# Optimization experiments

Hardware: AMD Instinct MI355X
Metric: run time of the kernel (lower is better)

## Reference

```python
import jax, jax.numpy as jnp
import numpy as np

N_NODES, N_EDGES, BATCH = 50000, 100000, 256
H = 64            # dim_hidden_features
D_NODE, D_EDGE, D_RBF = 110, 8, 8
D_SET = 2 * H     # Set2Set input_dim = 128, output_dim = 256
D_HID = 512
D_CAT = 54
MP_STEPS, S2S_ITERS = 4, 3


def setup_inputs() -> dict:
    key = jax.random.key(0)
    ks = iter(jax.random.split(key, 48))

    def nrm(shape, s=0.05):
        return jax.random.normal(next(ks), shape, dtype=jnp.float32) * s

    inp = {}
    inp["node_attribute"] = jax.random.normal(next(ks), (N_NODES, D_NODE), dtype=jnp.float32)
    inp["edge_attribute"] = jax.random.normal(next(ks), (N_EDGES, D_EDGE), dtype=jnp.float32)
    inp["edge_length"] = jax.random.uniform(next(ks), (N_EDGES,), dtype=jnp.float32)
    inp["src"] = jax.random.randint(next(ks), (N_EDGES,), 0, N_NODES, dtype=jnp.int32)
    inp["dst"] = jax.random.randint(next(ks), (N_EDGES,), 0, N_NODES, dtype=jnp.int32)
    inp["node_graph"] = jnp.sort(jax.random.randint(next(ks), (N_NODES,), 0, BATCH, dtype=jnp.int32))
    # atom_feature_projector
    inp["proj_W"] = nrm((D_NODE, H)); inp["proj_b"] = jnp.zeros((H,), jnp.float32)
    # RBF layer: centers ~ U(0,1), beta = 10 (per reset_parameters)
    inp["centers"] = jax.random.uniform(next(ks), (D_RBF,), dtype=jnp.float32)
    inp["beta"] = jnp.full((D_RBF,), 10.0, jnp.float32)
    # NNConv edge function: Linear(16 -> 64*64), plus NNConv bias
    inp["bond_W"] = nrm((D_EDGE + D_RBF, H * H)); inp["bond_b"] = jnp.zeros((H * H,), jnp.float32)
    inp["conv_b"] = jnp.zeros((H,), jnp.float32)
    # GRU (input H, hidden H); PyTorch layout (3H, in)
    inp["gru_Wih"] = nrm((3 * H, H)); inp["gru_Whh"] = nrm((3 * H, H))
    inp["gru_bih"] = jnp.zeros((3 * H,), jnp.float32); inp["gru_bhh"] = jnp.zeros((3 * H,), jnp.float32)
    # Set2Set LSTM: input 2*D_SET=256, hidden D_SET=128, 2 layers; PyTorch layout (4H, in)
    inp["lstm_Wih0"] = nrm((4 * D_SET, 2 * D_SET)); inp["lstm_Whh0"] = nrm((4 * D_SET, D_SET))
    inp["lstm_bih0"] = jnp.zeros((4 * D_SET,), jnp.float32); inp["lstm_bhh0"] = jnp.zeros((4 * D_SET,), jnp.float32)
    inp["lstm_Wih1"] = nrm((4 * D_SET, D_SET)); inp["lstm_Whh1"] = nrm((4 * D_SET, D_SET))
    inp["lstm_bih1"] = jnp.zeros((4 * D_SET,), jnp.float32); inp["lstm_bhh1"] = jnp.zeros((4 * D_SET,), jnp.float32)
    # sparsify: Linear(256 -> 512) + PReLU(init 0.25)
    inp["sp_W"] = nrm((2 * D_SET, D_HID)); inp["sp_b"] = jnp.zeros((D_HID,), jnp.float32)
    inp["prelu_a"] = jnp.array([0.25], jnp.float32)
    # catalyst1 head: hiddens[0] (512->512 ReLU, 512->512 Tanh) then outputs[0] (512->54)
    inp["h0_W1"] = nrm((D_HID, D_HID)); inp["h0_b1"] = jnp.zeros((D_HID,), jnp.float32)
    inp["h0_W2"] = nrm((D_HID, D_HID)); inp["h0_b2"] = jnp.zeros((D_HID,), jnp.float32)
    inp["out_W"] = nrm((D_HID, D_CAT)); inp["out_b"] = jnp.zeros((D_CAT,), jnp.float32)
    return inp


def _lstm_cell(x, h, c, Wih, Whh, bih, bhh):
    # PyTorch LSTM gate order: i, f, g, o
    g = x @ Wih.T + bih + h @ Whh.T + bhh
    i, f, gg, o = jnp.split(g, 4, axis=-1)
    c = jax.nn.sigmoid(f) * c + jax.nn.sigmoid(i) * jnp.tanh(gg)
    h = jax.nn.sigmoid(o) * jnp.tanh(c)
    return h, c


def reference(node_attribute, edge_attribute, edge_length, src, dst, node_graph,
              proj_W, proj_b, centers, beta, bond_W, bond_b, conv_b,
              gru_Wih, gru_Whh, gru_bih, gru_bhh,
              lstm_Wih0, lstm_Whh0, lstm_bih0, lstm_bhh0,
              lstm_Wih1, lstm_Whh1, lstm_bih1, lstm_bhh1,
              sp_W, sp_b, prelu_a, h0_W1, h0_b1, h0_W2, h0_b2, out_W, out_b):
    n_nodes = node_attribute.shape[0]
    # atom feature projection
    x = jax.nn.relu(node_attribute @ proj_W + proj_b)                       # (N, H)
    # edge features = [edge_attribute, RBF(length)]
    rbf = jnp.exp(-beta * (edge_length[:, None] - centers[None, :]) ** 2)   # (E, 8)
    efeat = jnp.concatenate([edge_attribute, rbf], axis=-1)                 # (E, 16)
    # NNConv per-edge weight matrix; edge features are constant over MP steps
    W_e = (efeat @ bond_W + bond_b).reshape(-1, H, H)                       # (E, H, H)

    feat, h = x, x
    for _ in range(MP_STEPS):
        # NNConv: message = h_src @ W_e, sum-aggregated at dst, plus bias
        m = jnp.einsum('ei,eio->eo', feat[src], W_e)                        # (E, H)
        agg = jax.ops.segment_sum(m, dst, num_segments=n_nodes) + conv_b    # (N, H)
        gx = jax.nn.relu(agg)
        # GRU cell (PyTorch gate order r, z, n)
        gi = gx @ gru_Wih.T + gru_bih
        gh = h @ gru_Whh.T + gru_bhh
        i_r, i_z, i_n = jnp.split(gi, 3, axis=-1)
        h_r, h_z, h_n = jnp.split(gh, 3, axis=-1)
        r = jax.nn.sigmoid(i_r + h_r)
        z = jax.nn.sigmoid(i_z + h_z)
        n = jnp.tanh(i_n + r * h_n)
        h = (1.0 - z) * n + z * h
        feat = h
    node_agg = jnp.concatenate([feat, x], axis=-1)                          # (N, 2H)

    # Set2Set pooling over graphs (segment softmax attention, 2-layer LSTM)
    B = BATCH
    h0 = c0 = jnp.zeros((B, D_SET), node_agg.dtype)
    h1 = c1 = jnp.zeros((B, D_SET), node_agg.dtype)
    q_star = jnp.zeros((B, 2 * D_SET), node_agg.dtype)
    for _ in range(S2S_ITERS):
        h0, c0 = _lstm_cell(q_star, h0, c0, lstm_Wih0, lstm_Whh0, lstm_bih0, lstm_bhh0)
        h1, c1 = _lstm_cell(h0, h1, c1, lstm_Wih1, lstm_Whh1, lstm_bih1, lstm_bhh1)
        q = h1                                                              # (B, 128)
        e = jnp.sum(node_agg * q[node_graph], axis=-1)                      # (N,)
        emax = jax.ops.segment_max(e, node_graph, num_segments=B)
        p = jnp.exp(e - emax[node_graph])
        denom = jax.ops.segment_sum(p, node_graph, num_segments=B)
        alpha = p / denom[node_graph]                                       # per-graph softmax
        r_out = jax.ops.segment_sum(node_agg * alpha[:, None], node_graph, num_segments=B)
        q_star = jnp.concatenate([q, r_out], axis=-1)                       # (B, 256)

    # sparsify (Linear + PReLU)
    feats = q_star @ sp_W + sp_b                                            # (B, 512)
    feats = jnp.where(feats >= 0, feats, prelu_a * feats)
    # catalyst1 head
    hid = jnp.tanh(jax.nn.relu(feats @ h0_W1 + h0_b1) @ h0_W2 + h0_b2)
    return jax.nn.softmax(hid @ out_W + out_b, axis=-1)                     # (B, 54)
```

## Files before the change

kernel.cpp:

```cpp
#include <hip/hip_runtime.h>
#include <math.h>

constexpr int N = 50000;
constexpr int E = 100000;
constexpr int B = 256;
constexpr int H = 64;
constexpr int DN = 110;
constexpr int NBLK = (E + 63) / 64;

#define DEV __device__ __forceinline__

typedef __attribute__((ext_vector_type(8))) short short8;
typedef __attribute__((ext_vector_type(4))) float floatx4;

DEV float sigf(float x) { return 1.0f / (1.0f + expf(-x)); }

DEV short f2bf(float f) {
    unsigned u = __float_as_uint(f);
    unsigned r = (u + 0x7fffu + ((u >> 16) & 1u)) >> 16;
    return (short)r;
}
DEV float bf2f(short s) { return __uint_as_float(((unsigned)(unsigned short)s) << 16); }

DEV void cvt8(const float* p, short8& hi, short8& lo) {
    float4 u0 = *(const float4*)p;
    float4 u1 = *(const float4*)(p + 4);
    float vv[8] = {u0.x, u0.y, u0.z, u0.w, u1.x, u1.y, u1.z, u1.w};
#pragma unroll
    for (int j = 0; j < 8; ++j) {
        short hb = f2bf(vv[j]);
        hi[j] = hb;
        lo[j] = f2bf(vv[j] - bf2f(hb));
    }
}

__global__ void k_izero(int* p, int n) {
    int i = blockIdx.x * 256 + threadIdx.x;
    if (i < n) p[i] = 0;
}

DEV void d_packpair(const float* __restrict__ in, float* __restrict__ out, int IN_I, int idx) {
    int i = idx >> 8;
    int j = idx & 255;
    out[2 * idx]     = in[(size_t)j * IN_I + i];
    out[2 * idx + 1] = in[(size_t)(j + 256) * IN_I + i];
}

DEV void d_prepB(const float* __restrict__ W, short* __restrict__ out,
                 int NT16, int ld, int trans, int ocap, int kcap, int idx) {
    int lane = idx & 63;
    int t = idx >> 6;
    int ntile = t % NT16;
    int kt = t / NT16;
    int quad = lane >> 4, col = lane & 15;
    int o = ntile * 16 + col;
    short hi[8], lo[8];
#pragma unroll
    for (int j = 0; j < 8; ++j) {
        int k = kt * 32 + quad * 8 + j;
        float v = 0.0f;
        if (o < ocap && k < kcap) v = trans ? W[(size_t)o * ld + k] : W[(size_t)k * ld + o];
        short hb = f2bf(v);
        hi[j] = hb;
        lo[j] = f2bf(v - bf2f(hb));
    }
    short* dh = out + (((size_t)(t * 2 + 0) * 64 + lane) * 8);
    short* dl = out + (((size_t)(t * 2 + 1) * 64 + lane) * 8);
#pragma unroll
    for (int j = 0; j < 8; ++j) { dh[j] = hi[j]; dl[j] = lo[j]; }
}

DEV void d_prepW(const float* __restrict__ bond_W, const float* __restrict__ bond_b,
                 short* __restrict__ wf, int idx) {
    int lane = idx & 63;
    int t = idx >> 6;
    int ks = t & 1;
    int nt = (t >> 1) & 3;
    int kk = t >> 3;
    const float* S = (kk < 16) ? (bond_W + kk * 4096) : bond_b;
    int quad = lane >> 4, col = lane & 15;
    short hi[8], lo[8];
#pragma unroll
    for (int j = 0; j < 8; ++j) {
        int i = ks * 32 + quad * 8 + j;
        float v = S[i * 64 + nt * 16 + col];
        short hb = f2bf(v);
        hi[j] = hb;
        lo[j] = f2bf(v - bf2f(hb));
    }
    short* dh = wf + (((size_t)(t * 2 + 0) * 64 + lane) * 8);
    short* dl = wf + (((size_t)(t * 2 + 1) * 64 + lane) * 8);
#pragma unroll
    for (int j = 0; j < 8; ++j) { dh[j] = hi[j]; dl[j] = lo[j]; }
}

__launch_bounds__(256)
__global__ void k_prep0(const float* lWih0, const float* lWhh0, const float* lWih1, const float* lWhh1,
                        float* lW0P, float* lU0P, float* lW1P, float* lU1P,
                        const float* bond_W, const float* bond_b, short* wf,
                        const float* gru_Wih, const float* gru_Whh, short* fgI, short* fgH,
                        const float* proj_W, short* fproj,
                        const float* ea, const float* el, const float* centers,
                        const float* beta, const int* epos, float* ef_t,
                        const int* ng, int* gs, int* ge) {
    int idx = blockIdx.x * 256 + threadIdx.x;
    if (idx < 65536) { d_packpair(lWih0, lW0P, 256, idx); return; }
    idx -= 65536;
    if (idx < 32768) { d_packpair(lWhh0, lU0P, 128, idx); return; }
    idx -= 32768;
    if (idx < 32768) { d_packpair(lWih1, lW1P, 128, idx); return; }
    idx -= 32768;
    if (idx < 32768) { d_packpair(lWhh1, lU1P, 128, idx); return; }
    idx -= 32768;
    if (idx < 8704) { d_prepW(bond_W, bond_b, wf, idx); return; }
    idx -= 8704;
    if (idx < 1536) { d_prepB(gru_Wih, fgI, 12, 64, 1, 192, 64, idx); return; }
    idx -= 1536;
    if (idx < 1536) { d_prepB(gru_Whh, fgH, 12, 64, 1, 192, 64, idx); return; }
    idx -= 1536;
    if (idx < 1024) { d_prepB(proj_W, fproj, 4, 64, 0, 64, DN, idx); return; }
    idx -= 1024;
    if (idx < E) {
        int e = idx;
        int pos = epos[e];
        float L = el[e];
#pragma unroll
        for (int j = 0; j < 8; ++j) ef_t[(size_t)j * E + pos] = ea[e * 8 + j];
#pragma unroll
        for (int j = 0; j < 8; ++j) {
            float d = L - centers[j];
            ef_t[(size_t)(8 + j) * E + pos] = expf(-beta[j] * d * d);
        }
        ef_t[(size_t)16 * E + pos] = 1.0f;
        return;
    }
    idx -= E;
    if (idx < N) {
        int n = idx;
        int g = ng[n];
        int gp = (n == 0) ? -1 : ng[n - 1];
        if (g != gp) {
            gs[g] = n;
            if (n > 0) ge[gp] = n;
            for (int q = gp + 1; q < g; ++q) { gs[q] = 0; ge[q] = 0; }
        }
        if (n == N - 1) {
            ge[g] = N;
            for (int q = g + 1; q < B; ++q) { gs[q] = 0; ge[q] = 0; }
        }
        return;
    }
}
constexpr int PREP0_TOTAL = 65536 + 3 * 32768 + 8704 + 2 * 1536 + 1024 + E + N;

__global__ void k_deg(const int* __restrict__ dst, int* __restrict__ deg) {
    int e = blockIdx.x * 256 + threadIdx.x;
    if (e < E) atomicAdd(&deg[dst[e]], 1);
}
__global__ void k_scan1(const int* __restrict__ deg, int* __restrict__ bsum) {
    __shared__ int s[256];
    int b = blockIdx.x, tid = threadIdx.x;
    int idx = b * 256 + tid;
    s[tid] = (idx < N) ? deg[idx] : 0;
    __syncthreads();
    for (int st = 128; st > 0; st >>= 1) {
        if (tid < st) s[tid] += s[tid + st];
        __syncthreads();
    }
    if (tid == 0) bsum[b] = s[0];
}
__global__ void k_scan2p(int* __restrict__ bsum, int nb) {
    __shared__ int s[256];
    int tid = threadIdx.x;
    int v = (tid < nb) ? bsum[tid] : 0;
    s[tid] = v;
    __syncthreads();
    for (int off = 1; off < 256; off <<= 1) {
        int t = (tid >= off) ? s[tid - off] : 0;
        __syncthreads();
        s[tid] += t;
        __syncthreads();
    }
    if (tid < nb) bsum[tid] = s[tid] - v;
}
__global__ void k_scan3(const int* __restrict__ deg, const int* __restrict__ bsum,
                        int* __restrict__ cursor, int* __restrict__ roff) {
    __shared__ int s[256];
    int b = blockIdx.x, tid = threadIdx.x;
    int idx = b * 256 + tid;
    int v = (idx < N) ? deg[idx] : 0;
    s[tid] = v;
    __syncthreads();
    for (int off = 1; off < 256; off <<= 1) {
        int t = (tid >= off) ? s[tid - off] : 0;
        __syncthreads();
        s[tid] += t;
        __syncthreads();
    }
    if (idx < N) {
        int start = bsum[b] + s[tid] - v;
        cursor[idx] = start;
        roff[idx] = start;
    }
    if (idx == 0) roff[N] = E;
}
__global__ void k_scat(const int* __restrict__ src, const int* __restrict__ dst,
                       int* __restrict__ cursor, int* __restrict__ srcp,
                       int* __restrict__ epos, int* __restrict__ dstp) {
    int e = blockIdx.x * 256 + threadIdx.x;
    if (e >= E) return;
    int d = dst[e];
    int pos = atomicAdd(&cursor[d], 1);
    srcp[pos] = src[e];
    dstp[pos] = d;
    epos[e] = pos;
}

__launch_bounds__(256)
__global__ void k_projm(const float* __restrict__ na, const short* __restrict__ fp,
                        const float* __restrict__ b, float* __restrict__ x,
                        short* __restrict__ hs) {
    __shared__ float as[16 * 132];
    int tid = threadIdx.x, lane = tid & 63, nt = tid >> 6;
    int quad = lane >> 4, col = lane & 15;
    int s0 = blockIdx.x * 16;
    for (int i = tid; i < 16 * DN; i += 256) {
        int r = i / DN, c = i % DN;
        as[r * 132 + c] = na[(size_t)s0 * DN + i];
    }
    for (int i = tid; i < 16 * 22; i += 256) {
        int r = i / 22, c = DN + i % 22;
        as[r * 132 + c] = 0.0f;
    }
    __syncthreads();
    const short8* F = (const short8*)fp;
    floatx4 T = {0.0f, 0.0f, 0.0f, 0.0f};
#pragma unroll
    for (int kt = 0; kt < 4; ++kt) {
        const float* ap = as + col * 132 + kt * 32 + quad * 8;
        short8 ah, al;
#pragma unroll
        for (int j = 0; j < 8; ++j) {
            float v = ap[j];
            short hb = f2bf(v);
            ah[j] = hb;
            al[j] = f2bf(v - bf2f(hb));
        }
        int t = kt * 4 + nt;
        short8 bh = F[(t * 2 + 0) * 64 + lane];
        short8 bl = F[(t * 2 + 1) * 64 + lane];
        T = __builtin_amdgcn_mfma_f32_16x16x32_bf16(ah, bh, T, 0, 0, 0);
        T = __builtin_amdgcn_mfma_f32_16x16x32_bf16(al, bh, T, 0, 0, 0);
        T = __builtin_amdgcn_mfma_f32_16x16x32_bf16(ah, bl, T, 0, 0, 0);
    }
    int o = nt * 16 + col;
    float bo = b[o];
#pragma unroll
    for (int r = 0; r < 4; ++r) {
        int n = s0 + quad * 4 + r;
        float v = fmaxf(T[r] + bo, 0.0f);
        x[(size_t)n * 64 + o] = v;
        short hb = f2bf(v);
        hs[(size_t)n * 128 + o] = hb;
        hs[(size_t)n * 128 + 64 + o] = f2bf(v - bf2f(hb));
    }
}

__launch_bounds__(256)
__global__ void k_msgagg(const short* __restrict__ hs, const float* __restrict__ ef_t,
                         const short* __restrict__ wf, const int* __restrict__ srcp,
                         const int* __restrict__ dstp,
                         float* __restrict__ agg, float* __restrict__ bpart) {
    __shared__ float efs[17 * 64];
    __shared__ int srcs[64];
    __shared__ int dsh[64];
    __shared__ int shprev;
    __shared__ float Csh[64][68];

    int tid = threadIdx.x;
    int e0 = blockIdx.x * 64;
    int lane = tid & 63;
    int nt = tid >> 6;
    int quad = lane >> 4, col = lane & 15;

    if (tid < 64) {
        int eg = e0 + tid;
        srcs[tid] = (eg < E) ? srcp[eg] : 0;
        dsh[tid] = (eg < E) ? dstp[eg] : N;
    }
    if (tid == 0) shprev = (e0 == 0) ? -1 : dstp[e0 - 1];
    for (int i = tid; i < 17 * 64; i += 256) {
        int kk = i >> 6, e = i & 63;
        int eg = e0 + e;
        efs[i] = (eg < E) ? ef_t[(size_t)kk * E + eg] : 0.0f;
    }
    __syncthreads();

    short8 Ah[4][2], Al[4][2];
#pragma unroll
    for (int mt = 0; mt < 4; ++mt) {
        int s = srcs[mt * 16 + col];
        const short* hp = hs + (size_t)s * 128 + quad * 8;
#pragma unroll
        for (int ks = 0; ks < 2; ++ks) {
            Ah[mt][ks] = *(const short8*)(hp + ks * 32);
            Al[mt][ks] = *(const short8*)(hp + 64 + ks * 32);
        }
    }

    const short8* Wf = (const short8*)wf;
    float C[4][4] = {};

#define LOADB(d0, d1, d2, d3, KK)                      \
    {                                                  \
        int tb_ = ((KK) * 4 + nt) * 2;                 \
        d0 = Wf[((tb_ + 0) * 2 + 0) * 64 + lane];      \
        d1 = Wf[((tb_ + 1) * 2 + 0) * 64 + lane];      \
        d2 = Wf[((tb_ + 0) * 2 + 1) * 64 + lane];      \
        d3 = Wf[((tb_ + 1) * 2 + 1) * 64 + lane];      \
    }

    short8 c0, c1, c2, c3, n0_, n1_, n2_, n3_, q0, q1, q2, q3;
    LOADB(c0, c1, c2, c3, 0);
    LOADB(n0_, n1_, n2_, n3_, 1);
    LOADB(q0, q1, q2, q3, 2);

#pragma unroll 1
    for (int kk = 0; kk < 17; ++kk) {
        int kn = kk + 3;
        if (kn > 16) kn = 16;
        short8 p0, p1, p2, p3;
        LOADB(p0, p1, p2, p3, kn);

#pragma unroll
        for (int mt = 0; mt < 4; ++mt) {
            floatx4 T = {0.0f, 0.0f, 0.0f, 0.0f};
            T = __builtin_amdgcn_mfma_f32_16x16x32_bf16(Ah[mt][0], c0, T, 0, 0, 0);
            T = __builtin_amdgcn_mfma_f32_16x16x32_bf16(Ah[mt][1], c1, T, 0, 0, 0);
            T = __builtin_amdgcn_mfma_f32_16x16x32_bf16(Al[mt][0], c0, T, 0, 0, 0);
            T = __builtin_amdgcn_mfma_f32_16x16x32_bf16(Al[mt][1], c1, T, 0, 0, 0);
            T = __builtin_amdgcn_mfma_f32_16x16x32_bf16(Ah[mt][0], c2, T, 0, 0, 0);
            T = __builtin_amdgcn_mfma_f32_16x16x32_bf16(Ah[mt][1], c3, T, 0, 0, 0);
            float4 ef = *(const float4*)&efs[kk * 64 + mt * 16 + quad * 4];
            C[mt][0] += ef.x * T[0];
            C[mt][1] += ef.y * T[1];
            C[mt][2] += ef.z * T[2];
            C[mt][3] += ef.w * T[3];
        }
        c0 = n0_; c1 = n1_; c2 = n2_; c3 = n3_;
        n0_ = q0; n1_ = q1; n2_ = q2; n3_ = q3;
        q0 = p0; q1 = p1; q2 = p2; q3 = p3;
    }
#undef LOADB

#pragma unroll
    for (int mt = 0; mt < 4; ++mt)
#pragma unroll
        for (int r = 0; r < 4; ++r)
            Csh[mt * 16 + quad * 4 + r][nt * 16 + col] = C[mt][r];
    __syncthreads();

    if (tid < 64) {
        int c = tid;
        int prevd = shprev;
        int firstd = dsh[0];
        for (int q = prevd + 1; q < firstd; ++q) agg[(size_t)q * 64 + c] = 0.0f;
        int cur = firstd;
        float acc = 0.0f;
        bool owned = (e0 == 0) || (firstd != prevd);
        bool done = false;
        for (int r = 0; r < 64; ++r) {
            int d = dsh[r];
            if (d != cur) {
                if (owned) agg[(size_t)cur * 64 + c] = acc;
                else bpart[(size_t)blockIdx.x * 64 + c] = acc;
                int dc = (d < N) ? d : N;
                for (int q = cur + 1; q < dc; ++q) agg[(size_t)q * 64 + c] = 0.0f;
                cur = d;
                acc = 0.0f;
                owned = true;
                if (cur >= N) { done = true; break; }
            }
            acc += Csh[r][c];
        }
        if (!done) {
            if (owned) agg[(size_t)cur * 64 + c] = acc;
            else bpart[(size_t)blockIdx.x * 64 + c] = acc;
        }
    }
}

__launch_bounds__(256)
__global__ void k_gru4(const float* agg, const float* __restrict__ bpart,
                       const int* __restrict__ roff, const float* __restrict__ conv_b,
                       short* __restrict__ hs,
                       const short* __restrict__ fI, const short* __restrict__ fH,
                       const float* __restrict__ bih, const float* __restrict__ bhh,
                       float* hf) {
    __shared__ float aggS[32 * 65];
    __shared__ short hsS[32 * 132];
    int tid = threadIdx.x, lane = tid & 63, nt = tid >> 6;
    int quad = lane >> 4, col = lane & 15;
    int n0 = blockIdx.x * 32;

    {
        const float* src = agg + (size_t)n0 * 64;
#pragma unroll
        for (int it = 0; it < 2; ++it) {
            int i = tid * 4 + it * 1024;
            float4 v = {0.0f, 0.0f, 0.0f, 0.0f};
            if ((size_t)n0 * 64 + i + 3 < (size_t)N * 64) v = *(const float4*)(src + i);
            int r = i >> 6, c = i & 63;
            *(float4*)&aggS[r * 65 + c] = v;
        }
        const short* hsrc = hs + (size_t)n0 * 128;
#pragma unroll
        for (int it = 0; it < 2; ++it) {
            int i = tid * 8 + it * 2048;
            short8 v = short8{0, 0, 0, 0, 0, 0, 0, 0};
            if ((size_t)n0 * 128 + i + 7 < (size_t)N * 128) v = *(const short8*)(hsrc + i);
            int r = i >> 7, c = i & 127;
            *(short8*)&hsS[r * 132 + c] = v;
        }
    }
    __syncthreads();

    short8 Gh[2][2], Gl[2][2], Hh[2][2], Hl[2][2];
#pragma unroll
    for (int mt = 0; mt < 2; ++mt) {
        int node = n0 + mt * 16 + col;
        bool ok = node < N;
        int row = mt * 16 + col;
        float acc[2][8];
        const float* ag = &aggS[row * 65];
#pragma unroll
        for (int ks = 0; ks < 2; ++ks) {
            const float* cb = conv_b + ks * 32 + quad * 8;
            float4 a0 = *(const float4*)(ag + ks * 32 + quad * 8);
            float4 a1 = *(const float4*)(ag + ks * 32 + quad * 8 + 4);
            acc[ks][0] = a0.x + cb[0]; acc[ks][1] = a0.y + cb[1];
            acc[ks][2] = a0.z + cb[2]; acc[ks][3] = a0.w + cb[3];
            acc[ks][4] = a1.x + cb[4]; acc[ks][5] = a1.y + cb[5];
            acc[ks][6] = a1.z + cb[6]; acc[ks][7] = a1.w + cb[7];
        }
        int rs = ok ? roff[node] : 0;
        int re = ok ? roff[node + 1] : 0;
        if (re > rs) {
            int b0 = rs >> 6, b1 = (re - 1) >> 6;
            for (int bb = b0 + 1; bb <= b1; ++bb) {
                const float* bp = bpart + (size_t)bb * 64;
#pragma unroll
                for (int ks = 0; ks < 2; ++ks) {
                    float4 p0 = *(const float4*)(bp + ks * 32 + quad * 8);
                    float4 p1 = *(const float4*)(bp + ks * 32 + quad * 8 + 4);
                    acc[ks][0] += p0.x; acc[ks][1] += p0.y;
                    acc[ks][2] += p0.z; acc[ks][3] += p0.w;
                    acc[ks][4] += p1.x; acc[ks][5] += p1.y;
                    acc[ks][6] += p1.z; acc[ks][7] += p1.w;
                }
            }
        }
        const short* hp = &hsS[row * 132];
#pragma unroll
        for (int ks = 0; ks < 2; ++ks) {
            Hh[mt][ks] = *(const short8*)(hp + ks * 32);
            Hl[mt][ks] = *(const short8*)(hp + 64 + ks * 32);
#pragma unroll
            for (int j = 0; j < 8; ++j) {
                float g = ok ? fmaxf(acc[ks][j], 0.0f) : 0.0f;
                short gb = f2bf(g);
                Gh[mt][ks][j] = gb;
                Gl[mt][ks][j] = f2bf(g - bf2f(gb));
            }
        }
    }
    __syncthreads();

    const short8* FI = (const short8*)fI;
    const short8* FH = (const short8*)fH;
    floatx4 aI[2][3] = {}, aH[2][3] = {};
#pragma unroll
    for (int ks = 0; ks < 2; ++ks) {
        short8 bIh[3], bIl[3], bHh[3], bHl[3];
#pragma unroll
        for (int g = 0; g < 3; ++g) {
            int t = ks * 12 + g * 4 + nt;
            bIh[g] = FI[(t * 2 + 0) * 64 + lane];
            bIl[g] = FI[(t * 2 + 1) * 64 + lane];
            bHh[g] = FH[(t * 2 + 0) * 64 + lane];
            bHl[g] = FH[(t * 2 + 1) * 64 + lane];
        }
#pragma unroll
        for (int mt = 0; mt < 2; ++mt) {
#pragma unroll
            for (int g = 0; g < 3; ++g) {
                aI[mt][g] = __builtin_amdgcn_mfma_f32_16x16x32_bf16(Gh[mt][ks], bIh[g], aI[mt][g], 0, 0, 0);
                aI[mt][g] = __builtin_amdgcn_mfma_f32_16x16x32_bf16(Gl[mt][ks], bIh[g], aI[mt][g], 0, 0, 0);
                aI[mt][g] = __builtin_amdgcn_mfma_f32_16x16x32_bf16(Gh[mt][ks], bIl[g], aI[mt][g], 0, 0, 0);
                aH[mt][g] = __builtin_amdgcn_mfma_f32_16x16x32_bf16(Hh[mt][ks], bHh[g], aH[mt][g], 0, 0, 0);
                aH[mt][g] = __builtin_amdgcn_mfma_f32_16x16x32_bf16(Hl[mt][ks], bHh[g], aH[mt][g], 0, 0, 0);
                aH[mt][g] = __builtin_amdgcn_mfma_f32_16x16x32_bf16(Hh[mt][ks], bHl[g], aH[mt][g], 0, 0, 0);
            }
        }
    }

    int o = nt * 16 + col;
    float br = bih[o], bz = bih[64 + o], bn = bih[128 + o];
    float cr = bhh[o], cz = bhh[64 + o], cn = bhh[128 + o];
#pragma unroll
    for (int mt = 0; mt < 2; ++mt) {
#pragma unroll
        for (int r = 0; r < 4; ++r) {
            int row = mt * 16 + quad * 4 + r;
            float rg = sigf(aI[mt][0][r] + br + aH[mt][0][r] + cr);
            float z  = sigf(aI[mt][1][r] + bz + aH[mt][1][r] + cz);
            float ng = tanhf(aI[mt][2][r] + bn + rg * (aH[mt][2][r] + cn));
            float hold = bf2f(hsS[row * 132 + o]) + bf2f(hsS[row * 132 + 64 + o]);
            aggS[row * 65 + o] = (1.0f - z) * ng + z * hold;
        }
    }
    __syncthreads();

#pragma unroll
    for (int it = 0; it < 2; ++it) {
        int i = tid * 8 + it * 2048;
        int r = i >> 7, c = i & 127;
        int node = n0 + r;
        if (node < N) {
            bool hiP = (c < 64);
            int f0 = hiP ? c : (c - 64);
            short8 v;
#pragma unroll
            for (int j = 0; j < 8; ++j) {
                float hv = aggS[r * 65 + f0 + j];
                short hb = f2bf(hv);
                v[j] = hiP ? hb : f2bf(hv - bf2f(hb));
            }
            *(short8*)(hs + (size_t)node * 128 + c) = v;
        }
    }
    if (hf) {
#pragma unroll
        for (int it = 0; it < 2; ++it) {
            int i = tid * 4 + it * 1024;
            int r = i >> 6, c = i & 63;
            int node = n0 + r;
            if (node < N)
                *(float4*)(hf + (size_t)node * 64 + c) = *(const float4*)&aggS[r * 65 + c];
        }
    }
}

__launch_bounds__(256)
__global__ void k_s2s3(float* __restrict__ q_star,
                       const float* __restrict__ W0P, const float* __restrict__ U0P,
                       const float* __restrict__ b0i, const float* __restrict__ b0h,
                       const float* __restrict__ W1P, const float* __restrict__ U1P,
                       const float* __restrict__ b1i, const float* __restrict__ b1h,
                       const float* __restrict__ hf, const float* __restrict__ x,
                       const int* __restrict__ gs, const int* __restrict__ ge,
                       const float* sp_W, short* fsp, const float* h0_W1, short* fw1,
                       const float* h0_W2, short* fw2, const float* out_W, short* fow) {
    __shared__ float xb[256], h0b[128], c0b[128], h1b[128], c1b[128];
    __shared__ float gb[512], h0n[128], qv[128];
    __shared__ float mrg[4][2][64];
    __shared__ float ml[4][2];
    int g = blockIdx.x, tid = threadIdx.x;
    int lane = tid & 63, grp = tid >> 6;
    int s0v = gs[g], s1v = ge[g];
    xb[tid] = 0.0f;
    if (tid < 128) { h0b[tid] = 0.0f; c0b[tid] = 0.0f; h1b[tid] = 0.0f; c1b[tid] = 0.0f; }
    __syncthreads();

    for (int it = 0; it < 3; ++it) {
        float g0 = b0i[tid] + b0h[tid];
        float g1 = b0i[tid + 256] + b0h[tid + 256];
        if (it > 0) {
            for (int i = 0; i < 256; ++i) {
                float xx = xb[i];
                float2 w = *(const float2*)(W0P + 2 * (i * 256 + tid));
                g0 += xx * w.x;
                g1 += xx * w.y;
            }
            for (int i = 0; i < 128; ++i) {
                float hh = h0b[i];
                float2 w = *(const float2*)(U0P + 2 * (i * 256 + tid));
                g0 += hh * w.x;
                g1 += hh * w.y;
            }
        }
        gb[tid] = g0; gb[tid + 256] = g1;
        __syncthreads();
        if (tid < 128) {
            float ii = gb[tid], ff = gb[128 + tid], gg = gb[256 + tid], oo = gb[384 + tid];
            float c = sigf(ff) * c0b[tid] + sigf(ii) * tanhf(gg);
            float hn = sigf(oo) * tanhf(c);
            c0b[tid] = c; h0b[tid] = hn; h0n[tid] = hn;
        }
        __syncthreads();
        float ga = b1i[tid] + b1h[tid];
        float gbv = b1i[tid + 256] + b1h[tid + 256];
        for (int i = 0; i < 128; ++i) {
            float xx = h0n[i];
            float2 w1 = *(const float2*)(W1P + 2 * (i * 256 + tid));
            ga += xx * w1.x;
            gbv += xx * w1.y;
        }
        if (it > 0) {
            for (int i = 0; i < 128; ++i) {
                float hh = h1b[i];
                float2 u1 = *(const float2*)(U1P + 2 * (i * 256 + tid));
                ga += hh * u1.x;
                gbv += hh * u1.y;
            }
        }
        gb[tid] = ga; gb[tid + 256] = gbv;
        __syncthreads();
        if (tid < 128) {
            float ii = gb[tid], ff = gb[128 + tid], gg = gb[256 + tid], oo = gb[384 + tid];
            float c = sigf(ff) * c1b[tid] + sigf(ii) * tanhf(gg);
            float hn = sigf(oo) * tanhf(c);
            c1b[tid] = c; h1b[tid] = hn; qv[tid] = hn;
        }
        __syncthreads();
        float qh = qv[lane], qx = qv[64 + lane];
        float mM = -INFINITY, lL = 0.0f, nh = 0.0f, nx = 0.0f;
        for (int n = s0v + grp; n < s1v; n += 16) {
            float hv[4], xv[4], e[4];
#pragma unroll
            for (int j = 0; j < 4; ++j) {
                int nj = n + 4 * j;
                int nc = (nj < s1v) ? nj : n;
                hv[j] = hf[(size_t)nc * 64 + lane];
                xv[j] = x[(size_t)nc * 64 + lane];
                e[j] = hv[j] * qh + xv[j] * qx;
            }
#pragma unroll
            for (int off = 32; off; off >>= 1) {
#pragma unroll
                for (int j = 0; j < 4; ++j) e[j] += __shfl_xor(e[j], off, 64);
            }
#pragma unroll
            for (int j = 0; j < 4; ++j)
                if (n + 4 * j >= s1v) e[j] = -INFINITY;
            float mb = fmaxf(fmaxf(e[0], e[1]), fmaxf(e[2], e[3]));
            float mn = fmaxf(mM, mb);
            float sc = expf(mM - mn);
            float w0 = expf(e[0] - mn), w1 = expf(e[1] - mn);
            float w2 = expf(e[2] - mn), w3 = expf(e[3] - mn);
            lL = lL * sc + ((w0 + w1) + (w2 + w3));
            nh = nh * sc + ((w0 * hv[0] + w1 * hv[1]) + (w2 * hv[2] + w3 * hv[3]));
            nx = nx * sc + ((w0 * xv[0] + w1 * xv[1]) + (w2 * xv[2] + w3 * xv[3]));
            mM = mn;
        }
        mrg[grp][0][lane] = nh;
        mrg[grp][1][lane] = nx;
        if (lane == 0) { ml[grp][0] = mM; ml[grp][1] = lL; }
        __syncthreads();
        if (tid < 128) {
            int half = tid >> 6, dl = tid & 63;
            float M = -INFINITY;
#pragma unroll
            for (int i = 0; i < 4; ++i) M = fmaxf(M, ml[i][0]);
            float L = 0.0f, NUM = 0.0f;
#pragma unroll
            for (int i = 0; i < 4; ++i) {
                float sc = expf(ml[i][0] - M);
                L += ml[i][1] * sc;
                NUM += mrg[i][half][dl] * sc;
            }
            xb[128 + tid] = (s1v > s0v) ? NUM / L : 0.0f;
            xb[tid] = qv[tid];
        }
        __syncthreads();
    }
    q_star[g * 256 + tid] = xb[tid];

    for (int ii2 = tid; ii2 < 336; ii2 += 256) {
        int idx = g * 336 + ii2;
        if (idx < 16384) { d_prepB(sp_W, fsp, 32, 512, 0, 512, 256, idx); continue; }
        idx -= 16384;
        if (idx < 32768) { d_prepB(h0_W1, fw1, 32, 512, 0, 512, 512, idx); continue; }
        idx -= 32768;
        if (idx < 32768) { d_prepB(h0_W2, fw2, 32, 512, 0, 512, 512, idx); continue; }
        idx -= 32768;
        d_prepB(out_W, fow, 4, 54, 0, 54, 512, idx);
    }
}

template<int MODE>
__launch_bounds__(256)
__global__ void k_hgemm(const float* __restrict__ A, const short* __restrict__ Bf,
                        const float* __restrict__ bias, const float* __restrict__ pa,
                        float* __restrict__ Cout, int K, int NT16) {
    int tid = threadIdx.x, lane = tid & 63, nt = tid >> 6;
    int quad = lane >> 4, col = lane & 15;
    int s0 = blockIdx.x * 16;
    int ntile = blockIdx.y * 4 + nt;
    int NoutTot = NT16 * 16;
    const short8* F = (const short8*)Bf;
    floatx4 T = {0.0f, 0.0f, 0.0f, 0.0f};
    const float* ap = A + (size_t)(s0 + col) * K + quad * 8;
    int KT = K >> 5;
#pragma unroll 4
    for (int kt = 0; kt < KT; ++kt) {
        short8 ah, al;
        cvt8(ap + kt * 32, ah, al);
        int t = kt * NT16 + ntile;
        short8 bh = F[(t * 2 + 0) * 64 + lane];
        short8 bl = F[(t * 2 + 1) * 64 + lane];
        T = __builtin_amdgcn_mfma_f32_16x16x32_bf16(ah, bh, T, 0, 0, 0);
        T = __builtin_amdgcn_mfma_f32_16x16x32_bf16(al, bh, T, 0, 0, 0);
        T = __builtin_amdgcn_mfma_f32_16x16x32_bf16(ah, bl, T, 0, 0, 0);
    }
    int o = ntile * 16 + col;
    float b = bias[o];
    float a = (MODE == 0) ? pa[0] : 0.0f;
#pragma unroll
    for (int r = 0; r < 4; ++r) {
        float v = T[r] + b;
        if (MODE == 0) v = (v >= 0.0f) ? v : a * v;
        if (MODE == 1) v = fmaxf(v, 0.0f);
        if (MODE == 2) v = tanhf(v);
        Cout[(size_t)(s0 + quad * 4 + r) * NoutTot + o] = v;
    }
}

__launch_bounds__(256)
__global__ void k_hout(const float* __restrict__ A, const short* __restrict__ Bf,
                       const float* __restrict__ ob, float* __restrict__ out) {
    __shared__ float sm[16][64];
    __shared__ float smax[16], sinv[16];
    int tid = threadIdx.x, lane = tid & 63, nt = tid >> 6;
    int quad = lane >> 4, col = lane & 15;
    int s0 = blockIdx.x * 16;
    const short8* F = (const short8*)Bf;
    floatx4 T = {0.0f, 0.0f, 0.0f, 0.0f};
    const float* ap = A + (size_t)(s0 + col) * 512 + quad * 8;
#pragma unroll 4
    for (int kt = 0; kt < 16; ++kt) {
        short8 ah, al;
        cvt8(ap + kt * 32, ah, al);
        int t = kt * 4 + nt;
        short8 bh = F[(t * 2 + 0) * 64 + lane];
        short8 bl = F[(t * 2 + 1) * 64 + lane];
        T = __builtin_amdgcn_mfma_f32_16x16x32_bf16(ah, bh, T, 0, 0, 0);
        T = __builtin_amdgcn_mfma_f32_16x16x32_bf16(al, bh, T, 0, 0, 0);
        T = __builtin_amdgcn_mfma_f32_16x16x32_bf16(ah, bl, T, 0, 0, 0);
    }
    int o = nt * 16 + col;
    float b = (o < 54) ? ob[o] : 0.0f;
#pragma unroll
    for (int r = 0; r < 4; ++r)
        sm[quad * 4 + r][o] = (o < 54) ? (T[r] + b) : -1e30f;
    __syncthreads();
    if (tid < 16) {
        float m = -INFINITY;
        for (int j = 0; j < 54; ++j) m = fmaxf(m, sm[tid][j]);
        float s = 0.0f;
        for (int j = 0; j < 54; ++j) s += expf(sm[tid][j] - m);
        smax[tid] = m;
        sinv[tid] = 1.0f / s;
    }
    __syncthreads();
    for (int idx = tid; idx < 16 * 54; idx += 256) {
        int srow = idx / 54, oo = idx % 54;
        out[(size_t)(s0 + srow) * 54 + oo] = expf(sm[srow][oo] - smax[srow]) * sinv[srow];
    }
}

extern "C" void kernel_launch(void* const* d_in, const int* in_sizes, int n_in,
                              void* d_out, int out_size, void* d_ws, size_t ws_size,
                              hipStream_t stream) {
    const float* node_attr = (const float*)d_in[0];
    const float* edge_attr = (const float*)d_in[1];
    const float* edge_len  = (const float*)d_in[2];
    const int*   src       = (const int*)d_in[3];
    const int*   dst       = (const int*)d_in[4];
    const int*   node_grph = (const int*)d_in[5];
    const float* proj_W    = (const float*)d_in[6];
    const float* proj_b    = (const float*)d_in[7];
    const float* centers   = (const float*)d_in[8];
    const float* beta      = (const float*)d_in[9];
    const float* bond_W    = (const float*)d_in[10];
    const float* bond_b    = (const float*)d_in[11];
    const float* conv_b    = (const float*)d_in[12];
    const float* gru_Wih   = (const float*)d_in[13];
    const float* gru_Whh   = (const float*)d_in[14];
    const float* gru_bih   = (const float*)d_in[15];
    const float* gru_bhh   = (const float*)d_in[16];
    const float* lWih0     = (const float*)d_in[17];
    const float* lWhh0     = (const float*)d_in[18];
    const float* lbih0     = (const float*)d_in[19];
    const float* lbhh0     = (const float*)d_in[20];
    const float* lWih1     = (const float*)d_in[21];
    const float* lWhh1     = (const float*)d_in[22];
    const float* lbih1     = (const float*)d_in[23];
    const float* lbhh1     = (const float*)d_in[24];
    const float* sp_W      = (const float*)d_in[25];
    const float* sp_b      = (const float*)d_in[26];
    const float* prelu_a   = (const float*)d_in[27];
    const float* h0_W1     = (const float*)d_in[28];
    const float* h0_b1     = (const float*)d_in[29];
    const float* h0_W2     = (const float*)d_in[30];
    const float* h0_b2     = (const float*)d_in[31];
    const float* out_W     = (const float*)d_in[32];
    const float* out_b     = (const float*)d_in[33];
    float* out = (float*)d_out;

    float* ws = (float*)d_ws;
    size_t off = 0;
    float* x      = ws + off; off += (size_t)N * 64;
    float* hsf    = ws + off; off += (size_t)N * 64;
    float* ef_t   = ws + off; off += (size_t)E * 17;
    float* agg    = ws + off; off += (size_t)N * 64;
    float* wfrag  = ws + off; off += 17 * 16 * 64 * 8 / 2;
    float* fgI    = ws + off; off += 2 * 64 * 192 / 2;
    float* fgH    = ws + off; off += 2 * 64 * 192 / 2;
    float* fproj  = ws + off; off += 16 * 1024 / 2;
    float* lW0P   = ws + off; off += 256 * 512;
    float* lU0P   = ws + off; off += 128 * 512;
    float* lW1P   = ws + off; off += 128 * 512;
    float* lU1P   = ws + off; off += 128 * 512;
    float* q_star = ws + off; off += B * 256;
    float* bpart  = ws + off; off += (size_t)NBLK * 64;
    int* gs       = (int*)(ws + off); off += B;
    int* ge       = (int*)(ws + off); off += B;
    int* deg      = (int*)(ws + off); off += N;
    int* cursor   = (int*)(ws + off); off += N;
    int* roff     = (int*)(ws + off); off += N + 1;
    int* bsum     = (int*)(ws + off); off += 256;
    int* srcp     = (int*)(ws + off); off += E;
    int* epos     = (int*)(ws + off); off += E;
    int* dstp     = (int*)(ws + off); off += E;

    short* hs = (short*)hsf;

    short* fsp = (short*)ef_t;
    short* fw1 = (short*)(ef_t + 131072);
    short* fw2 = (short*)(ef_t + 131072 + 262144);
    short* fow = (short*)(ef_t + 131072 + 2 * 262144);
    float* hb1 = ef_t + 131072 + 2 * 262144 + 32768;
    float* hb2 = hb1 + 131072;

    constexpr int NB = (N + 255) / 256;

    k_izero<<<NB, 256, 0, stream>>>(deg, N);
    k_deg<<<(E + 255) / 256, 256, 0, stream>>>(dst, deg);
    k_scan1<<<NB, 256, 0, stream>>>(deg, bsum);
    k_scan2p<<<1, 256, 0, stream>>>(bsum, NB);
    k_scan3<<<NB, 256, 0, stream>>>(deg, bsum, cursor, roff);
    k_scat<<<(E + 255) / 256, 256, 0, stream>>>(src, dst, cursor, srcp, epos, dstp);

    k_prep0<<<(PREP0_TOTAL + 255) / 256, 256, 0, stream>>>(
        lWih0, lWhh0, lWih1, lWhh1, lW0P, lU0P, lW1P, lU1P,
        bond_W, bond_b, (short*)wfrag, gru_Wih, gru_Whh, (short*)fgI, (short*)fgH,
        proj_W, (short*)fproj,
        edge_attr, edge_len, centers, beta, epos, ef_t,
        node_grph, gs, ge);

    k_projm<<<N / 16, 256, 0, stream>>>(node_attr, (const short*)fproj, proj_b, x, hs);

    for (int step = 0; step < 4; ++step) {
        k_msgagg<<<NBLK, 256, 0, stream>>>(hs, ef_t, (const short*)wfrag, srcp, dstp,
                                           agg, bpart);
        k_gru4<<<(N + 31) / 32, 256, 0, stream>>>(agg, bpart, roff, conv_b, hs,
                                                  (const short*)fgI, (const short*)fgH,
                                                  gru_bih, gru_bhh,
                                                  (step == 3) ? agg : nullptr);
    }

    k_s2s3<<<B, 256, 0, stream>>>(q_star,
                                  lW0P, lU0P, lbih0, lbhh0,
                                  lW1P, lU1P, lbih1, lbhh1,
                                  agg, x, gs, ge,
                                  sp_W, fsp, h0_W1, fw1, h0_W2, fw2, out_W, fow);

    k_hgemm<0><<<dim3(16, 8), 256, 0, stream>>>(q_star, fsp, sp_b, prelu_a, hb1, 256, 32);
    k_hgemm<1><<<dim3(16, 8), 256, 0, stream>>>(hb1, fw1, h0_b1, nullptr, hb2, 512, 32);
    k_hgemm<2><<<dim3(16, 8), 256, 0, stream>>>(hb2, fw2, h0_b2, nullptr, hb1, 512, 32);
    k_hout<<<16, 256, 0, stream>>>(hb1, fow, out_b, out);
}
```

Baseline: 671.2 us.

## Double Set2Set block to 512 threads with one LSTM gate per thread

The Set2Set kernel now launches 512 threads per graph instead of 256. Each thread computes a single LSTM gate output from a plainly transposed weight matrix, rather than two gates from pair-packed weights. The attention pass over nodes runs with 8 wave groups instead of 4, which halves the serial node loop per wave. The aim is more parallelism in this latency-bound, single-block-per-graph kernel. The cost is more block-wide sync overhead and a prep kernel that now uses an uncoalesced scatter transpose.

```diff
diff --git a/kernel.cpp b/kernel.cpp
--- a/kernel.cpp
+++ b/kernel.cpp
@@ -39,11 +39,9 @@
     if (i < n) p[i] = 0;
 }
 
-DEV void d_packpair(const float* __restrict__ in, float* __restrict__ out, int IN_I, int idx) {
-    int i = idx >> 8;
-    int j = idx & 255;
-    out[2 * idx]     = in[(size_t)j * IN_I + i];
-    out[2 * idx + 1] = in[(size_t)(j + 256) * IN_I + i];
+DEV void d_transpose(const float* in, float* out, int R, int C, int idx) {
+    int r = idx / C, c = idx % C;
+    out[c * R + r] = in[idx];
 }
 
 DEV void d_prepB(const float* __restrict__ W, short* __restrict__ out,
@@ -96,7 +94,7 @@
 
 __launch_bounds__(256)
 __global__ void k_prep0(const float* lWih0, const float* lWhh0, const float* lWih1, const float* lWhh1,
-                        float* lW0P, float* lU0P, float* lW1P, float* lU1P,
+                        float* lW0T, float* lU0T, float* lW1T, float* lU1T,
                         const float* bond_W, const float* bond_b, short* wf,
                         const float* gru_Wih, const float* gru_Whh, short* fgI, short* fgH,
                         const float* proj_W, short* fproj,
@@ -104,14 +102,14 @@
                         const float* beta, const int* epos, float* ef_t,
                         const int* ng, int* gs, int* ge) {
     int idx = blockIdx.x * 256 + threadIdx.x;
-    if (idx < 65536) { d_packpair(lWih0, lW0P, 256, idx); return; }
+    if (idx < 131072) { d_transpose(lWih0, lW0T, 512, 256, idx); return; }
+    idx -= 131072;
+    if (idx < 65536) { d_transpose(lWhh0, lU0T, 512, 128, idx); return; }
     idx -= 65536;
-    if (idx < 32768) { d_packpair(lWhh0, lU0P, 128, idx); return; }
-    idx -= 32768;
-    if (idx < 32768) { d_packpair(lWih1, lW1P, 128, idx); return; }
-    idx -= 32768;
-    if (idx < 32768) { d_packpair(lWhh1, lU1P, 128, idx); return; }
-    idx -= 32768;
+    if (idx < 65536) { d_transpose(lWih1, lW1T, 512, 128, idx); return; }
+    idx -= 65536;
+    if (idx < 65536) { d_transpose(lWhh1, lU1T, 512, 128, idx); return; }
+    idx -= 65536;
     if (idx < 8704) { d_prepW(bond_W, bond_b, wf, idx); return; }
     idx -= 8704;
     if (idx < 1536) { d_prepB(gru_Wih, fgI, 12, 64, 1, 192, 64, idx); return; }
@@ -151,7 +149,7 @@
         return;
     }
 }
-constexpr int PREP0_TOTAL = 65536 + 3 * 32768 + 8704 + 2 * 1536 + 1024 + E + N;
+constexpr int PREP0_TOTAL = 131072 + 3 * 65536 + 8704 + 2 * 1536 + 1024 + E + N;
 
 __global__ void k_deg(const int* __restrict__ dst, int* __restrict__ deg) {
     int e = blockIdx.x * 256 + threadIdx.x;
@@ -551,11 +549,11 @@
     }
 }
 
-__launch_bounds__(256)
+__launch_bounds__(512)
 __global__ void k_s2s3(float* __restrict__ q_star,
-                       const float* __restrict__ W0P, const float* __restrict__ U0P,
+                       const float* __restrict__ W0T, const float* __restrict__ U0T,
                        const float* __restrict__ b0i, const float* __restrict__ b0h,
-                       const float* __restrict__ W1P, const float* __restrict__ U1P,
+                       const float* __restrict__ W1T, const float* __restrict__ U1T,
                        const float* __restrict__ b1i, const float* __restrict__ b1h,
                        const float* __restrict__ hf, const float* __restrict__ x,
                        const int* __restrict__ gs, const int* __restrict__ ge,
@@ -563,33 +561,24 @@
                        const float* h0_W2, short* fw2, const float* out_W, short* fow) {
     __shared__ float xb[256], h0b[128], c0b[128], h1b[128], c1b[128];
     __shared__ float gb[512], h0n[128], qv[128];
-    __shared__ float mrg[4][2][64];
-    __shared__ float ml[4][2];
+    __shared__ float mrg[8][2][64];
+    __shared__ float ml[8][2];
     int g = blockIdx.x, tid = threadIdx.x;
     int lane = tid & 63, grp = tid >> 6;
     int s0v = gs[g], s1v = ge[g];
-    xb[tid] = 0.0f;
+    if (tid < 256) xb[tid] = 0.0f;
     if (tid < 128) { h0b[tid] = 0.0f; c0b[tid] = 0.0f; h1b[tid] = 0.0f; c1b[tid] = 0.0f; }
     __syncthreads();
 
     for (int it = 0; it < 3; ++it) {
         float g0 = b0i[tid] + b0h[tid];
-        float g1 = b0i[tid + 256] + b0h[tid + 256];
         if (it > 0) {
-            for (int i = 0; i < 256; ++i) {
-                float xx = xb[i];
-                float2 w = *(const float2*)(W0P + 2 * (i * 256 + tid));
-                g0 += xx * w.x;
-                g1 += xx * w.y;
-            }
-            for (int i = 0; i < 128; ++i) {
-                float hh = h0b[i];
-                float2 w = *(const float2*)(U0P + 2 * (i * 256 + tid));
-                g0 += hh * w.x;
-                g1 += hh * w.y;
-            }
-        }
-        gb[tid] = g0; gb[tid + 256] = g1;
+#pragma unroll 4
+            for (int i = 0; i < 256; ++i) g0 += xb[i] * W0T[i * 512 + tid];
+#pragma unroll 4
+            for (int i = 0; i < 128; ++i) g0 += h0b[i] * U0T[i * 512 + tid];
+        }
+        gb[tid] = g0;
         __syncthreads();
         if (tid < 128) {
             float ii = gb[tid], ff = gb[128 + tid], gg = gb[256 + tid], oo = gb[384 + tid];
@@ -599,22 +588,13 @@
         }
         __syncthreads();
         float ga = b1i[tid] + b1h[tid];
-        float gbv = b1i[tid + 256] + b1h[tid + 256];
-        for (int i = 0; i < 128; ++i) {
-            float xx = h0n[i];
-            float2 w1 = *(const float2*)(W1P + 2 * (i * 256 + tid));
-            ga += xx * w1.x;
-            gbv += xx * w1.y;
-        }
+#pragma unroll 4
+        for (int i = 0; i < 128; ++i) ga += h0n[i] * W1T[i * 512 + tid];
         if (it > 0) {
-            for (int i = 0; i < 128; ++i) {
-                float hh = h1b[i];
-                float2 u1 = *(const float2*)(U1P + 2 * (i * 256 + tid));
-                ga += hh * u1.x;
-                gbv += hh * u1.y;
-            }
-        }
-        gb[tid] = ga; gb[tid + 256] = gbv;
+#pragma unroll 4
+            for (int i = 0; i < 128; ++i) ga += h1b[i] * U1T[i * 512 + tid];
+        }
+        gb[tid] = ga;
         __syncthreads();
         if (tid < 128) {
             float ii = gb[tid], ff = gb[128 + tid], gg = gb[256 + tid], oo = gb[384 + tid];
@@ -625,11 +605,11 @@
         __syncthreads();
         float qh = qv[lane], qx = qv[64 + lane];
         float mM = -INFINITY, lL = 0.0f, nh = 0.0f, nx = 0.0f;
-        for (int n = s0v + grp; n < s1v; n += 16) {
+        for (int n = s0v + grp; n < s1v; n += 32) {
             float hv[4], xv[4], e[4];
 #pragma unroll
             for (int j = 0; j < 4; ++j) {
-                int nj = n + 4 * j;
+                int nj = n + 8 * j;
                 int nc = (nj < s1v) ? nj : n;
                 hv[j] = hf[(size_t)nc * 64 + lane];
                 xv[j] = x[(size_t)nc * 64 + lane];
@@ -642,7 +622,7 @@
             }
 #pragma unroll
             for (int j = 0; j < 4; ++j)
-                if (n + 4 * j >= s1v) e[j] = -INFINITY;
+                if (n + 8 * j >= s1v) e[j] = -INFINITY;
             float mb = fmaxf(fmaxf(e[0], e[1]), fmaxf(e[2], e[3]));
             float mn = fmaxf(mM, mb);
             float sc = expf(mM - mn);
@@ -661,10 +641,10 @@
             int half = tid >> 6, dl = tid & 63;
             float M = -INFINITY;
 #pragma unroll
-            for (int i = 0; i < 4; ++i) M = fmaxf(M, ml[i][0]);
+            for (int i = 0; i < 8; ++i) M = fmaxf(M, ml[i][0]);
             float L = 0.0f, NUM = 0.0f;
 #pragma unroll
-            for (int i = 0; i < 4; ++i) {
+            for (int i = 0; i < 8; ++i) {
                 float sc = expf(ml[i][0] - M);
                 L += ml[i][1] * sc;
                 NUM += mrg[i][half][dl] * sc;
@@ -674,9 +654,9 @@
         }
         __syncthreads();
     }
-    q_star[g * 256 + tid] = xb[tid];
-
-    for (int ii2 = tid; ii2 < 336; ii2 += 256) {
+    if (tid < 256) q_star[g * 256 + tid] = xb[tid];
+
+    for (int ii2 = tid; ii2 < 336; ii2 += 512) {
         int idx = g * 336 + ii2;
         if (idx < 16384) { d_prepB(sp_W, fsp, 32, 512, 0, 512, 256, idx); continue; }
         idx -= 16384;
@@ -818,10 +798,10 @@
     float* fgI    = ws + off; off += 2 * 64 * 192 / 2;
     float* fgH    = ws + off; off += 2 * 64 * 192 / 2;
     float* fproj  = ws + off; off += 16 * 1024 / 2;
-    float* lW0P   = ws + off; off += 256 * 512;
-    float* lU0P   = ws + off; off += 128 * 512;
-    float* lW1P   = ws + off; off += 128 * 512;
-    float* lU1P   = ws + off; off += 128 * 512;
+    float* lW0T   = ws + off; off += 256 * 512;
+    float* lU0T   = ws + off; off += 128 * 512;
+    float* lW1T   = ws + off; off += 128 * 512;
+    float* lU1T   = ws + off; off += 128 * 512;
     float* q_star = ws + off; off += B * 256;
     float* bpart  = ws + off; off += (size_t)NBLK * 64;
     int* gs       = (int*)(ws + off); off += B;
@@ -853,7 +833,7 @@
     k_scat<<<(E + 255) / 256, 256, 0, stream>>>(src, dst, cursor, srcp, epos, dstp);
 
     k_prep0<<<(PREP0_TOTAL + 255) / 256, 256, 0, stream>>>(
-        lWih0, lWhh0, lWih1, lWhh1, lW0P, lU0P, lW1P, lU1P,
+        lWih0, lWhh0, lWih1, lWhh1, lW0T, lU0T, lW1T, lU1T,
         bond_W, bond_b, (short*)wfrag, gru_Wih, gru_Whh, (short*)fgI, (short*)fgH,
         proj_W, (short*)fproj,
         edge_attr, edge_len, centers, beta, epos, ef_t,
@@ -870,9 +850,9 @@
                                                   (step == 3) ? agg : nullptr);
     }
 
-    k_s2s3<<<B, 256, 0, stream>>>(q_star,
-                                  lW0P, lU0P, lbih0, lbhh0,
-                                  lW1P, lU1P, lbih1, lbhh1,
+    k_s2s3<<<B, 512, 0, stream>>>(q_star,
+                                  lW0T, lU0T, lbih0, lbhh0,
+                                  lW1T, lU1T, lbih1, lbhh1,
                                   agg, x, gs, ge,
                                   sp_W, fsp, h0_W1, fw1, h0_W2, fw2, out_W, fow);
 
```

Result: slower. 717.2 us (+6.8%).
